# Optimization experiments

Hardware: AMD Instinct MI355X
Metric: run time of the kernel (lower is better)

The kernel has to match this reference:

```python
import jax, jax.numpy as jnp
import numpy as np

B, C, N_IN = 32, 64, 10475
N_OUT = 2619
NNZ = 8 * N_OUT  # ~8 barycentric entries per output vertex


def setup_inputs() -> dict:
    key = jax.random.key(0)
    k1, k2, k3, k4 = jax.random.split(key, 4)
    x = jax.random.normal(k1, (B, C, N_IN), dtype=jnp.float32)
    # Sparse mesh-sampling operator M [N_OUT, N_IN] in COO form,
    # sparsity pattern shared across the whole batch.
    M_rows = jax.random.randint(k2, (NNZ,), 0, N_OUT, dtype=jnp.int32)
    M_cols = jax.random.randint(k3, (NNZ,), 0, N_IN, dtype=jnp.int32)
    M_vals = jax.random.uniform(k4, (NNZ,), dtype=jnp.float32)
    return {"x": x, "M_rows": M_rows, "M_cols": M_cols, "M_vals": M_vals}


def reference(x, M_rows, M_cols, M_vals):
    """Batched spmm: out[b, c, r] = sum_{k: M_rows[k]==r} M_vals[k] * x[b, c, M_cols[k]].

    Equivalent to the torch module: for each batch element, M @ x[b].T, stacked,
    then transposed back to [B, C, N_OUT]. Here the batch loop is fused into a
    single gather + segment_sum that reuses the shared sparsity pattern.
    """
    # Gather source vertex features for every nnz entry: [B, C, NNZ]
    g = x[:, :, M_cols] * M_vals
    # segment_sum reduces over the leading axis -> move nnz to front
    g = jnp.moveaxis(g, 2, 0)                                   # [NNZ, B, C]
    out = jax.ops.segment_sum(g, M_rows, num_segments=N_OUT)    # [N_OUT, B, C]
    return jnp.moveaxis(out, 0, 2)                              # [B, C, N_OUT]
```

## Files before the change

kernel.cpp:

```cpp
#include <hip/hip_runtime.h>
#include <hip/hip_fp16.h>
#include <stdint.h>

#define Bdim   32
#define Cdim   64
#define N_IN   10475
#define N_OUT  2619
#define NNZ    (8 * N_OUT)
#define MAIN_BLK 512
#define CHUNK  41
#define SMALL_BLK 256
#define Gpair  2
#define NBLK   (Bdim * Cdim / Gpair)

#define PAIR_FULL 10
#define PAIR_TAIL 117

#define SENT_META 0x0FFF0000u

#define OFF_ENT    0
#define OFF_ELAST  (OFF_ENT + 20 * MAIN_BLK * 16)
#define OFF_CUR    (OFF_ELAST + MAIN_BLK * 8)
#define OFF_OFFS   (OFF_CUR + 10480)
#define WS_NEEDED  (OFF_OFFS + 10496)

static __device__ __forceinline__ uint32_t pack_h2(float a, float b) {
    __half2 h = __float22half2_rn(make_float2(a, b));
    return *(uint32_t*)&h;
}
static __device__ __forceinline__ float2 unpack_h2(uint32_t u) {
    __half2 h = *(__half2*)&u;
    return __half22float2(h);
}

#define HS_BLK 1024
__global__ __launch_bounds__(HS_BLK) void hist_scan(
        const int* __restrict__ rows,
        int* __restrict__ cursor, int* __restrict__ offsets) {
    __shared__ int cnt[N_OUT];
    __shared__ int wsum[16];
    const int t = threadIdx.x, lane = t & 63, w = t >> 6;

    for (int i = t; i < N_OUT; i += HS_BLK) cnt[i] = 0;
    __syncthreads();

    const int4* __restrict__ r4 = (const int4*)rows;
    #pragma unroll
    for (int i = t; i < NNZ / 4; i += HS_BLK) {
        int4 v = r4[i];
        atomicAdd(&cnt[v.x], 1);
        atomicAdd(&cnt[v.y], 1);
        atomicAdd(&cnt[v.z], 1);
        atomicAdd(&cnt[v.w], 1);
    }
    __syncthreads();

    const int base = t * 3;
    int v0 = (base + 0 < N_OUT) ? cnt[base + 0] : 0;
    int v1 = (base + 1 < N_OUT) ? cnt[base + 1] : 0;
    int v2 = (base + 2 < N_OUT) ? cnt[base + 2] : 0;
    int s = v0 + v1 + v2;
    const int tot = s;
    #pragma unroll
    for (int d = 1; d < 64; d <<= 1) {
        int n = __shfl_up(s, d);
        if (lane >= d) s += n;
    }
    if (lane == 63) wsum[w] = s;
    __syncthreads();
    if (t < 16) {
        int ws_ = wsum[t];
        #pragma unroll
        for (int d = 1; d < 16; d <<= 1) {
            int n = __shfl_up(ws_, d);
            if (t >= d) ws_ += n;
        }
        wsum[t] = ws_;
    }
    __syncthreads();
    int excl = ((w > 0) ? wsum[w - 1] : 0) + (s - tot);
    if (base + 0 <= N_OUT) { offsets[base + 0] = excl; if (base + 0 < N_OUT) cursor[base + 0] = excl; }
    excl += v0;
    if (base + 1 <= N_OUT) { offsets[base + 1] = excl; if (base + 1 < N_OUT) cursor[base + 1] = excl; }
    excl += v1;
    if (base + 2 <= N_OUT) { offsets[base + 2] = excl; if (base + 2 < N_OUT) cursor[base + 2] = excl; }
}

__global__ __launch_bounds__(SMALL_BLK) void scatter_entries(
        const int* __restrict__ rows, const int* __restrict__ cols,
        const float* __restrict__ vals,
        int* __restrict__ cursor, const int* __restrict__ offsets,
        uint2* __restrict__ ent2, uint2* __restrict__ entLast) {
    const int t = threadIdx.x;
    if (blockIdx.x == 0 && t >= 1 && t <= 40) {
        uint2 e = make_uint2(SENT_META, 0u);
        if (t < 40) ent2[(t >> 1) * (MAIN_BLK * 2) + 511 * 2 + (t & 1)] = e;
        else        entLast[511] = e;
    }
    int k = blockIdx.x * SMALL_BLK + t;
    if (k < NNZ) {
        int r = rows[k];
        int p = atomicAdd(&cursor[r], 1);
        uint32_t flag = (p == offsets[r + 1] - 1) ? 0x80000000u : 0u;
        uint32_t meta = flag | ((uint32_t)r << 16) | ((uint32_t)cols[k] << 2);
        uint2 e = make_uint2(meta, __float_as_uint(vals[k]));
        int tt = p / CHUNK;
        int ss = p - tt * CHUNK;
        if (ss < 40) ent2[(ss >> 1) * (MAIN_BLK * 2) + tt * 2 + (ss & 1)] = e;
        else         entLast[tt] = e;
    }
}

__global__ __launch_bounds__(MAIN_BLK, 6) void spmm_g2h(
        const float* __restrict__ x,
        const uint4* __restrict__ ent4,
        const uint2* __restrict__ entLast,
        float* __restrict__ out) {
    __shared__ uint32_t xs[N_IN];
    __shared__ uint32_t out2[N_OUT];
    __shared__ int      wCarryRow[8];
    __shared__ float    wC0[8], wC1[8];

    const int blk  = blockIdx.x;
    const int t    = threadIdx.x, lane = t & 63, w = t >> 6;
    const float* __restrict__ xr0 = x + (size_t)(Gpair * blk) * N_IN;
    const float* __restrict__ xr1 = xr0 + N_IN;

    {
        const float2* __restrict__ x0v = (const float2*)xr0;
        const float2* __restrict__ x1v = (const float2*)(xr1 + 1);
        __half* __restrict__ xl = (__half*)xs;
        #pragma unroll
        for (int k = 0; k < PAIR_FULL; ++k) {
            int i = t + k * MAIN_BLK;
            float2 a = x0v[i];
            float2 b = x1v[i];
            xl[4 * i + 0] = __float2half(a.x);
            xl[4 * i + 2] = __float2half(a.y);
            xl[4 * i + 3] = __float2half(b.x);
            xl[4 * i + 5] = __float2half(b.y);
        }
        if (t < PAIR_TAIL) {
            int i = PAIR_FULL * MAIN_BLK + t;
            float2 a = x0v[i];
            float2 b = x1v[i];
            xl[4 * i + 0] = __float2half(a.x);
            xl[4 * i + 2] = __float2half(a.y);
            xl[4 * i + 3] = __float2half(b.x);
            xl[4 * i + 5] = __float2half(b.y);
        }
        if (t == MAIN_BLK - 1) {
            xl[2 * (N_IN - 1)] = __float2half(xr0[N_IN - 1]);
            xl[1]              = __float2half(xr1[0]);
        }
    }
    #pragma unroll
    for (int i = t; i < N_OUT; i += MAIN_BLK) out2[i] = 0u;
    __syncthreads();

    float acc0 = 0.f, acc1 = 0.f, f0 = 0.f, f1 = 0.f;
    int firstRow = -1;

#define FEED(meta, vb) do {                                              \
        uint32_t xp = xs[((meta) & 0xFFFFu) >> 2];                       \
        float v = __uint_as_float(vb);                                   \
        float2 xf = unpack_h2(xp);                                       \
        acc0 = fmaf(v, xf.x, acc0);                                      \
        acc1 = fmaf(v, xf.y, acc1);                                      \
        if ((int)(meta) < 0) {                                           \
            int row_ = (int)(((meta) >> 16) & 0xFFFu);                   \
            if (firstRow < 0) { firstRow = row_; f0 = acc0; f1 = acc1; } \
            else out2[row_] = pack_h2(acc0, acc1);                       \
            acc0 = 0.f; acc1 = 0.f;                                      \
        }                                                                \
    } while (0)

    uint2 el = entLast[t];
    uint4 c0 = ent4[0 * MAIN_BLK + t];
    uint4 c1 = ent4[1 * MAIN_BLK + t];
    uint4 c2 = ent4[2 * MAIN_BLK + t];
    uint4 c3 = ent4[3 * MAIN_BLK + t];

    #pragma unroll
    for (int jb = 0; jb < 5; ++jb) {
        uint4 n0, n1, n2, n3;
        if (jb < 4) {
            n0 = ent4[((jb + 1) * 4 + 0) * MAIN_BLK + t];
            n1 = ent4[((jb + 1) * 4 + 1) * MAIN_BLK + t];
            n2 = ent4[((jb + 1) * 4 + 2) * MAIN_BLK + t];
            n3 = ent4[((jb + 1) * 4 + 3) * MAIN_BLK + t];
        }
        FEED(c0.x, c0.y); FEED(c0.z, c0.w);
        FEED(c1.x, c1.y); FEED(c1.z, c1.w);
        FEED(c2.x, c2.y); FEED(c2.z, c2.w);
        FEED(c3.x, c3.y); FEED(c3.z, c3.w);
        if (jb < 4) { c0 = n0; c1 = n1; c2 = n2; c3 = n3; }
    }
    FEED(el.x, el.y);
#undef FEED

    const int   carryRow = (int)((el.x >> 16) & 0xFFFu);
    const float cc0 = acc0, cc1 = acc1;

    int   pRow = __shfl_up(carryRow, 1);
    float p0   = __shfl_up(cc0, 1);
    float p1   = __shfl_up(cc1, 1);
    if (lane == 63) { wCarryRow[w] = carryRow; wC0[w] = cc0; wC1[w] = cc1; }
    __syncthreads();
    if (lane == 0) {
        pRow = (w > 0) ? wCarryRow[w - 1] : -1;
        p0   = (w > 0) ? wC0[w - 1] : 0.f;
        p1   = (w > 0) ? wC1[w - 1] : 0.f;
    }

    if (firstRow >= 0 && firstRow < N_OUT) {
        bool m = (pRow == firstRow);
        out2[firstRow] = pack_h2(f0 + (m ? p0 : 0.f), f1 + (m ? p1 : 0.f));
    }
    __syncthreads();

    float* __restrict__ o0 = out + (size_t)(Gpair * blk) * N_OUT;
    float* __restrict__ o1 = o0 + N_OUT;
    #pragma unroll
    for (int i = t; i < N_OUT; i += MAIN_BLK) {
        float2 vv = unpack_h2(out2[i]);
        o0[i] = vv.x;
        o1[i] = vv.y;
    }
}

__global__ __launch_bounds__(SMALL_BLK) void spmm_raw(
        const float* __restrict__ x,
        const int* __restrict__ rows,
        const int* __restrict__ cols,
        const float* __restrict__ vals,
        float* __restrict__ out) {
    __shared__ float x_lds[N_IN];
    __shared__ float out_lds[N_OUT];
    const int bc = blockIdx.x;
    const float* __restrict__ xrow = x + (size_t)bc * N_IN;
    for (int i = threadIdx.x; i < N_IN; i += SMALL_BLK) x_lds[i] = xrow[i];
    for (int i = threadIdx.x; i < N_OUT; i += SMALL_BLK) out_lds[i] = 0.0f;
    __syncthreads();
    for (int k = threadIdx.x; k < NNZ; k += SMALL_BLK) {
        atomicAdd(&out_lds[rows[k]], vals[k] * x_lds[cols[k]]);
    }
    __syncthreads();
    float* __restrict__ orow = out + (size_t)bc * N_OUT;
    for (int i = threadIdx.x; i < N_OUT; i += SMALL_BLK) orow[i] = out_lds[i];
}

extern "C" void kernel_launch(void* const* d_in, const int* in_sizes, int n_in,
                              void* d_out, int out_size, void* d_ws, size_t ws_size,
                              hipStream_t stream) {
    const float* x    = (const float*)d_in[0];
    const int*   rows = (const int*)d_in[1];
    const int*   cols = (const int*)d_in[2];
    const float* vals = (const float*)d_in[3];
    float*       out  = (float*)d_out;

    if (ws_size >= (size_t)WS_NEEDED) {
        char*  ws      = (char*)d_ws;
        uint2* ent2    = (uint2*)(ws + OFF_ENT);
        const uint4* ent4 = (const uint4*)(ws + OFF_ENT);
        uint2* entLast = (uint2*)(ws + OFF_ELAST);
        int*   cursor  = (int*)(ws + OFF_CUR);
        int*   offsets = (int*)(ws + OFF_OFFS);

        const int gk = (NNZ + SMALL_BLK - 1) / SMALL_BLK;

        hist_scan<<<1, HS_BLK, 0, stream>>>(rows, cursor, offsets);
        scatter_entries<<<gk, SMALL_BLK, 0, stream>>>(rows, cols, vals, cursor,
                                                      offsets, ent2, entLast);
        spmm_g2h<<<NBLK, MAIN_BLK, 0, stream>>>(x, ent4, entLast, out);
    } else {
        spmm_raw<<<Bdim * Cdim, SMALL_BLK, 0, stream>>>(x, rows, cols, vals, out);
    }
}
```

Before: 152.2 us.

## Double spmm block size and halve per-thread chunk with segmented carry scan

Doubles the main kernel's block size to 1024 threads and halves the entries each thread processes (CHUNK 41 to 21), so the x-to-half conversion and the entry walk are spread over more threads. Because a row can now span several short chunks, the single-neighbour carry fix-up is replaced by a segmented prefix scan within and across wavefronts. Sentinel padding in the scatter kernel is generalised to fill all unused slots. The extra scan and synchronisation add overhead, and larger blocks may limit how many blocks share an SM alongside the shared-memory footprint.

```diff
diff --git a/kernel.cpp b/kernel.cpp
--- a/kernel.cpp
+++ b/kernel.cpp
@@ -7,19 +7,20 @@
 #define N_IN   10475
 #define N_OUT  2619
 #define NNZ    (8 * N_OUT)
-#define MAIN_BLK 512
-#define CHUNK  41
+#define MAIN_BLK 1024
+#define CHUNK  21
+#define NSLOT  (MAIN_BLK * CHUNK)
 #define SMALL_BLK 256
 #define Gpair  2
 #define NBLK   (Bdim * Cdim / Gpair)
 
-#define PAIR_FULL 10
+#define PAIR_FULL 5
 #define PAIR_TAIL 117
 
 #define SENT_META 0x0FFF0000u
 
 #define OFF_ENT    0
-#define OFF_ELAST  (OFF_ENT + 20 * MAIN_BLK * 16)
+#define OFF_ELAST  (OFF_ENT + 10 * MAIN_BLK * 16)
 #define OFF_CUR    (OFF_ELAST + MAIN_BLK * 8)
 #define OFF_OFFS   (OFF_CUR + 10480)
 #define WS_NEEDED  (OFF_OFFS + 10496)
@@ -92,10 +93,18 @@
         int* __restrict__ cursor, const int* __restrict__ offsets,
         uint2* __restrict__ ent2, uint2* __restrict__ entLast) {
     const int t = threadIdx.x;
-    if (blockIdx.x == 0 && t >= 1 && t <= 40) {
-        uint2 e = make_uint2(SENT_META, 0u);
-        if (t < 40) ent2[(t >> 1) * (MAIN_BLK * 2) + 511 * 2 + (t & 1)] = e;
-        else        entLast[511] = e;
+    if (blockIdx.x == 0) {
+        #pragma unroll
+        for (int j = 0; j < 3; ++j) {
+            int p = NNZ + j * SMALL_BLK + t;
+            if (p < NSLOT) {
+                int tt = p / CHUNK;
+                int ss = p - tt * CHUNK;
+                uint2 e = make_uint2(SENT_META, 0u);
+                if (ss < 20) ent2[(ss >> 1) * (MAIN_BLK * 2) + tt * 2 + (ss & 1)] = e;
+                else         entLast[tt] = e;
+            }
+        }
     }
     int k = blockIdx.x * SMALL_BLK + t;
     if (k < NNZ) {
@@ -106,20 +115,20 @@
         uint2 e = make_uint2(meta, __float_as_uint(vals[k]));
         int tt = p / CHUNK;
         int ss = p - tt * CHUNK;
-        if (ss < 40) ent2[(ss >> 1) * (MAIN_BLK * 2) + tt * 2 + (ss & 1)] = e;
-        else         entLast[tt] = e;
-    }
-}
-
-__global__ __launch_bounds__(MAIN_BLK, 6) void spmm_g2h(
+        if (ss < 40 && ss < 20) ent2[(ss >> 1) * (MAIN_BLK * 2) + tt * 2 + (ss & 1)] = e;
+        else                    entLast[tt] = e;
+    }
+}
+
+__global__ __launch_bounds__(MAIN_BLK, 8) void spmm_g2h(
         const float* __restrict__ x,
         const uint4* __restrict__ ent4,
         const uint2* __restrict__ entLast,
         float* __restrict__ out) {
     __shared__ uint32_t xs[N_IN];
     __shared__ uint32_t out2[N_OUT];
-    __shared__ int      wCarryRow[8];
-    __shared__ float    wC0[8], wC1[8];
+    __shared__ int      wM[16], wRow[16];
+    __shared__ float    wB0[16], wB1[16], wS0[16], wS1[16];
 
     const int blk  = blockIdx.x;
     const int t    = threadIdx.x, lane = t & 63, w = t >> 6;
@@ -154,7 +163,6 @@
             xl[1]              = __float2half(xr1[0]);
         }
     }
-    #pragma unroll
     for (int i = t; i < N_OUT; i += MAIN_BLK) out2[i] = 0u;
     __syncthreads();
 
@@ -178,50 +186,74 @@
     uint2 el = entLast[t];
     uint4 c0 = ent4[0 * MAIN_BLK + t];
     uint4 c1 = ent4[1 * MAIN_BLK + t];
-    uint4 c2 = ent4[2 * MAIN_BLK + t];
-    uint4 c3 = ent4[3 * MAIN_BLK + t];
 
     #pragma unroll
     for (int jb = 0; jb < 5; ++jb) {
-        uint4 n0, n1, n2, n3;
+        uint4 n0, n1;
         if (jb < 4) {
-            n0 = ent4[((jb + 1) * 4 + 0) * MAIN_BLK + t];
-            n1 = ent4[((jb + 1) * 4 + 1) * MAIN_BLK + t];
-            n2 = ent4[((jb + 1) * 4 + 2) * MAIN_BLK + t];
-            n3 = ent4[((jb + 1) * 4 + 3) * MAIN_BLK + t];
+            n0 = ent4[((jb + 1) * 2 + 0) * MAIN_BLK + t];
+            n1 = ent4[((jb + 1) * 2 + 1) * MAIN_BLK + t];
         }
         FEED(c0.x, c0.y); FEED(c0.z, c0.w);
         FEED(c1.x, c1.y); FEED(c1.z, c1.w);
-        FEED(c2.x, c2.y); FEED(c2.z, c2.w);
-        FEED(c3.x, c3.y); FEED(c3.z, c3.w);
-        if (jb < 4) { c0 = n0; c1 = n1; c2 = n2; c3 = n3; }
+        if (jb < 4) { c0 = n0; c1 = n1; }
     }
     FEED(el.x, el.y);
 #undef FEED
 
-    const int   carryRow = (int)((el.x >> 16) & 0xFFFu);
-    const float cc0 = acc0, cc1 = acc1;
-
-    int   pRow = __shfl_up(carryRow, 1);
-    float p0   = __shfl_up(cc0, 1);
-    float p1   = __shfl_up(cc1, 1);
-    if (lane == 63) { wCarryRow[w] = carryRow; wC0[w] = cc0; wC1[w] = cc1; }
-    __syncthreads();
+    const int r_last = (int)((el.x >> 16) & 0xFFFu);
+    int   sm  = (firstRow >= 0) ? 0 : 1;
+    float sb0 = acc0, sb1 = acc1;
+
+    #pragma unroll
+    for (int d = 1; d < 64; d <<= 1) {
+        int   pm = __shfl_up(sm, d);
+        float p0 = __shfl_up(sb0, d);
+        float p1 = __shfl_up(sb1, d);
+        if (lane >= d) {
+            if (sm) { sb0 += p0; sb1 += p1; }
+            sm &= pm;
+        }
+    }
+    if (lane == 63) { wM[w] = sm; wB0[w] = sb0; wB1[w] = sb1; wRow[w] = r_last; }
+    __syncthreads();
+    if (t < 16) {
+        int m2 = wM[t];
+        float b20 = wB0[t], b21 = wB1[t];
+        #pragma unroll
+        for (int d = 1; d < 16; d <<= 1) {
+            int   qm = __shfl_up(m2, d);
+            float q0 = __shfl_up(b20, d);
+            float q1 = __shfl_up(b21, d);
+            if (t >= d) {
+                if (m2) { b20 += q0; b21 += q1; }
+                m2 &= qm;
+            }
+        }
+        wS0[t] = b20; wS1[t] = b21;
+    }
+    __syncthreads();
+
+    const float Bx0 = (w > 0) ? wS0[w - 1] : 0.f;
+    const float Bx1 = (w > 0) ? wS1[w - 1] : 0.f;
+    float Si0 = sb0 + (sm ? Bx0 : 0.f);
+    float Si1 = sb1 + (sm ? Bx1 : 0.f);
+    float Sp0 = __shfl_up(Si0, 1);
+    float Sp1 = __shfl_up(Si1, 1);
+    int   prevRow = __shfl_up(r_last, 1);
     if (lane == 0) {
-        pRow = (w > 0) ? wCarryRow[w - 1] : -1;
-        p0   = (w > 0) ? wC0[w - 1] : 0.f;
-        p1   = (w > 0) ? wC1[w - 1] : 0.f;
+        Sp0 = Bx0; Sp1 = Bx1;
+        prevRow = (w > 0) ? wRow[w - 1] : -1;
     }
 
     if (firstRow >= 0 && firstRow < N_OUT) {
-        bool m = (pRow == firstRow);
-        out2[firstRow] = pack_h2(f0 + (m ? p0 : 0.f), f1 + (m ? p1 : 0.f));
+        bool m = (prevRow == firstRow);
+        out2[firstRow] = pack_h2(f0 + (m ? Sp0 : 0.f), f1 + (m ? Sp1 : 0.f));
     }
     __syncthreads();
 
     float* __restrict__ o0 = out + (size_t)(Gpair * blk) * N_OUT;
     float* __restrict__ o1 = o0 + N_OUT;
-    #pragma unroll
     for (int i = t; i < N_OUT; i += MAIN_BLK) {
         float2 vv = unpack_h2(out2[i]);
         o0[i] = vv.x;
```

After: 153.4 us. Within noise of the previous version (+0.8%).
